# Performance work log

Measured on AMD Instinct MI355X. Metric: run time of the kernel, lower is better.

Reference implementation:

```python
import jax, jax.numpy as jnp
import numpy as np

STRIDE = (1, 1, 1)  # (h_stride, w_stride, d_stride)
# padding order in module: (left,right,up,down,forward,backward) -> h, w, d dims
PAD = ((1, 1), (1, 1), (1, 1))  # ((pad_left,pad_right) on h, (up,down) on w, (fwd,bwd) on d)


def setup_inputs() -> dict:
    key = jax.random.key(0)
    k1, k2, k3 = jax.random.split(key, 3)
    X = jax.random.normal(k1, (4, 32, 32, 64, 64), dtype=jnp.float32)        # (B, Cin, h, w, d)
    weight = jax.random.normal(k2, (64, 32, 3, 3, 3), dtype=jnp.float32) * 0.5  # (Cout, Cin, kh, kw, kd)
    bias = jax.random.normal(k3, (64,), dtype=jnp.float32) * 0.5
    return {"X": X, "weight": weight, "bias": bias}


def _conv3d(X, weight, bias):
    # cross-correlation conv3d, identical math to the nested-loop MAC in MyConv3d
    y = jax.lax.conv_general_dilated(
        X, weight,
        window_strides=STRIDE,
        padding=PAD,
        dimension_numbers=("NCHWD", "OIHWD", "NCHWD"),
    )
    return y + bias[None, :, None, None, None]


def reference(X, weight, bias):
    return _conv3d(X, weight, bias)
```

## Files before the change

### kernel.cpp

```cpp
#include <hip/hip_runtime.h>
#include <hip/hip_bf16.h>

typedef __attribute__((ext_vector_type(8))) short bf16x8;
typedef __attribute__((ext_vector_type(4))) float f32x4;
typedef __attribute__((ext_vector_type(4))) unsigned int u32x4;

#define B_N   4
#define C_IN  32
#define C_OUT 64
#define S_H   32
#define S_W   64
#define S_D   64
#define HWD   (S_H * S_W * S_D)

#define WPK_USHORTS     (4 * 28 * 64 * 8)
#define WS_NEEDED       ((size_t)WPK_USHORTS * 2 + 64)

__device__ __forceinline__ ushort f2bf(float f) {
    unsigned u = __builtin_bit_cast(unsigned, f);
    unsigned r = (u + 0x7FFFu + ((u >> 16) & 1u)) >> 16;
    return (ushort)r;
}

__device__ __forceinline__ unsigned cvt_pk(float lo, float hi) {
    unsigned r;
    asm("v_cvt_pk_bf16_f32 %0, %1, %2" : "=v"(r) : "v"(lo), "v"(hi));
    return r;
}

typedef const __attribute__((address_space(1))) unsigned int* dma_gptr;
typedef __attribute__((address_space(3))) unsigned int* dma_lptr;

__device__ __forceinline__ void dma16(const void* g, void* l) {
    __builtin_amdgcn_global_load_lds((dma_gptr)g, (dma_lptr)l, 16, 0, 0);
}

__device__ __forceinline__ void pin_load(float& dst, const float* p) {
    asm volatile("global_load_dword %0, %1, off" : "=v"(dst) : "v"(p));
}

__global__ __launch_bounds__(256) void pack_w_kernel(
    const float* __restrict__ Wt, ushort* __restrict__ Wpk, float* __restrict__ Zpf)
{
    int idx = blockIdx.x * 256 + threadIdx.x;
    int cic = idx / 1792;
    int r   = idx - cic * 1792;
    int tap = r >> 6;
    int co  = r & 63;
    bf16x8 pk;
    #pragma unroll
    for (int j = 0; j < 8; ++j)
        pk[j] = (tap < 27) ? (short)f2bf(Wt[((long)co * C_IN + cic * 8 + j) * 27 + tap])
                           : (short)0;
    *((bf16x8*)Wpk + idx) = pk;
    if (blockIdx.x == 0 && threadIdx.x < 16) Zpf[threadIdx.x] = 0.f;
}

__global__ __launch_bounds__(256, 2) void conv3d_fused_kernel(
    const float* __restrict__ X, const ushort* __restrict__ Wpk,
    const float* __restrict__ Zpf,
    const float* __restrict__ bias, float* __restrict__ out)
{
    __shared__ ushort Xs[1188 * 8];
    __shared__ ushort Ws[1792 * 8];

    const int tid  = threadIdx.x;
    const int lane = tid & 63;
    const int wave = tid >> 6;
    const int nl   = lane & 15;
    const int quad = lane >> 4;

    const int blk = blockIdx.x;
    const int wt  = blk & 15;
    const int h   = (blk >> 4) & 31;
    const int b   = blk >> 9;
    const int w0  = wt * 4;

    const int cs = ((blk >> 3) + (blk >> 8)) & 3;

    const float* xb[5];
    int adv[5];
    #pragma unroll
    for (int k = 0; k < 5; ++k) {
        int s = tid + k * 256;
        xb[k] = Zpf; adv[k] = 0;
        if (s < 1188) {
            int hh   = s / 396;
            int r0   = s - hh * 396;
            int ww   = r0 / 66;
            int dpos = r0 - ww * 66;
            int hp  = h - 1 + hh;
            int wp2 = w0 - 1 + ww;
            int dp  = dpos - 1;
            bool ok = (unsigned)hp < S_H && (unsigned)wp2 < S_W && (unsigned)dp < S_D;
            if (ok) {
                xb[k]  = X + ((((long)b * C_IN) * S_H + hp) * S_W + wp2) * S_D + dp;
                adv[k] = HWD;
            }
        }
    }

    int a_off[7], b_off[7];
    #pragma unroll
    for (int tg = 0; tg < 7; ++tg) {
        int tap = tg * 4 + quad;
        int tb  = tap < 27 ? tap : 0;
        int kh = tb / 9;
        int r9 = tb - kh * 9;
        int kw = r9 / 3;
        int kd = r9 - kw * 3;
        a_off[tg] = (tap * 64 + nl) * 8;
        b_off[tg] = (((kh * 6 + kw + wave) * 66) + kd + nl) * 8;
    }

    float bs[16];
    #pragma unroll
    for (int mi = 0; mi < 4; ++mi)
        #pragma unroll
        for (int r = 0; r < 4; ++r)
            bs[mi * 4 + r] = bias[mi * 16 + quad * 4 + r];

    f32x4 acc[16];
    #pragma unroll
    for (int i = 0; i < 16; ++i) acc[i] = (f32x4){0.f, 0.f, 0.f, 0.f};

    float xv[5][8];

    #pragma unroll
    for (int k = 0; k < 5; ++k) {
        int s = tid + k * 256;
        if (s < 1188) {
            #pragma unroll
            for (int j = 0; j < 8; ++j)
                pin_load(xv[k][j], xb[k] + (long)(cs * 8 + j) * adv[k]);
        }
    }
    __builtin_amdgcn_sched_barrier(0);
    {
        const ushort* src = Wpk + (long)cs * 1792 * 8;
        #pragma unroll
        for (int k = 0; k < 7; ++k) {
            int s = tid + k * 256;
            dma16(src + s * 8, &Ws[s * 8]);
        }
    }
    __builtin_amdgcn_sched_barrier(0);
    asm volatile("s_waitcnt vmcnt(7)" ::: "memory");
    __builtin_amdgcn_sched_barrier(0);
    #pragma unroll
    for (int k = 0; k < 5; ++k) {
        int s = tid + k * 256;
        if (s < 1188) {
            u32x4 pk;
            #pragma unroll
            for (int j = 0; j < 4; ++j)
                pk[j] = cvt_pk(xv[k][2 * j], xv[k][2 * j + 1]);
            *(u32x4*)&Xs[s * 8] = pk;
        }
    }

    for (int cic = 0; cic < 4; ++cic) {
        __syncthreads();

        const int cn = (cic + 1 + cs) & 3;
        if (cic < 3) {
            #pragma unroll
            for (int k = 0; k < 5; ++k) {
                int s = tid + k * 256;
                if (s < 1188) {
                    #pragma unroll
                    for (int j = 0; j < 8; ++j)
                        pin_load(xv[k][j], xb[k] + (long)(cn * 8 + j) * adv[k]);
                }
            }
        }
        __builtin_amdgcn_sched_barrier(0);

        #pragma unroll
        for (int tg = 0; tg < 7; ++tg) {
            bf16x8 af[4], bf[4];
            #pragma unroll
            for (int mi = 0; mi < 4; ++mi)
                af[mi] = *(const bf16x8*)&Ws[a_off[tg] + mi * 128];
            #pragma unroll
            for (int dt = 0; dt < 4; ++dt)
                bf[dt] = *(const bf16x8*)&Xs[b_off[tg] + dt * 128];
            __builtin_amdgcn_s_setprio(1);
            #pragma unroll
            for (int mi = 0; mi < 4; ++mi)
                #pragma unroll
                for (int dt = 0; dt < 4; ++dt)
                    acc[mi * 4 + dt] = __builtin_amdgcn_mfma_f32_16x16x32_bf16(
                        af[mi], bf[dt], acc[mi * 4 + dt], 0, 0, 0);
            __builtin_amdgcn_s_setprio(0);
        }

        if (cic < 3) {
            __syncthreads();
            asm volatile("s_waitcnt vmcnt(0)" ::: "memory");
            __builtin_amdgcn_sched_barrier(0);

            {
                const ushort* src = Wpk + (long)cn * 1792 * 8;
                #pragma unroll
                for (int k = 0; k < 7; ++k) {
                    int s = tid + k * 256;
                    dma16(src + s * 8, &Ws[s * 8]);
                }
            }
            #pragma unroll
            for (int k = 0; k < 5; ++k) {
                int s = tid + k * 256;
                if (s < 1188) {
                    u32x4 pk;
                    #pragma unroll
                    for (int j = 0; j < 4; ++j)
                        pk[j] = cvt_pk(xv[k][2 * j], xv[k][2 * j + 1]);
                    *(u32x4*)&Xs[s * 8] = pk;
                }
            }
        }
    }

    const int w = w0 + wave;
    #pragma unroll
    for (int mi = 0; mi < 4; ++mi) {
        #pragma unroll
        for (int dt = 0; dt < 4; ++dt) {
            f32x4 a = acc[mi * 4 + dt];
            int d0 = dt * 16 + nl;
            #pragma unroll
            for (int r = 0; r < 4; ++r) {
                int co = mi * 16 + quad * 4 + r;
                out[(((long)(b * C_OUT + co) * S_H + h) * S_W + w) * S_D + d0]
                    = a[r] + bs[mi * 4 + r];
            }
        }
    }
}

__global__ __launch_bounds__(256) void conv3d_mfma_fallback(
    const float* __restrict__ X, const float* __restrict__ Wt,
    const float* __restrict__ bias, float* __restrict__ out)
{
    __shared__ ushort Xs[3 * 6 * 66 * 8];
    __shared__ ushort Ws[28 * 64 * 8];

    const int tid  = threadIdx.x;
    const int lane = tid & 63;
    const int wave = tid >> 6;
    const int nl   = lane & 15;
    const int quad = lane >> 4;
    const int co_base = wave * 16;

    const int blk = blockIdx.x;
    const int wt  = blk & 15;
    const int h   = (blk >> 4) & 31;
    const int b   = blk >> 9;
    const int w0  = wt * 4;

    float bs[4];
    #pragma unroll
    for (int r = 0; r < 4; ++r) bs[r] = bias[co_base + quad * 4 + r];

    f32x4 acc[16];
    #pragma unroll
    for (int i = 0; i < 16; ++i) acc[i] = (f32x4){0.f, 0.f, 0.f, 0.f};

    for (int cic = 0; cic < 4; ++cic) {
        __syncthreads();
        for (int s = tid; s < 64 * 27; s += 256) {
            int co = s / 27;
            int t  = s - co * 27;
            const float* wp = Wt + ((long)co * C_IN + cic * 8) * 27 + t;
            bf16x8 pk;
            #pragma unroll
            for (int j = 0; j < 8; ++j) pk[j] = (short)f2bf(wp[j * 27]);
            *(bf16x8*)&Ws[(t * 64 + co) * 8] = pk;
        }
        for (int s = tid; s < 64; s += 256) {
            bf16x8 z;
            #pragma unroll
            for (int j = 0; j < 8; ++j) z[j] = 0;
            *(bf16x8*)&Ws[(27 * 64 + s) * 8] = z;
        }
        for (int s = tid; s < 1188; s += 256) {
            int hh   = s / 396;
            int r0   = s - hh * 396;
            int ww   = r0 / 66;
            int dpos = r0 - ww * 66;
            int hp = h - 1 + hh;
            int wp2 = w0 - 1 + ww;
            int dp = dpos - 1;
            bool ok = (unsigned)hp < S_H && (unsigned)wp2 < S_W && (unsigned)dp < S_D;
            int hc = min(max(hp, 0), S_H - 1);
            int wc = min(max(wp2, 0), S_W - 1);
            int dc = min(max(dp, 0), S_D - 1);
            const float* xp = X + (((long)(b * C_IN + cic * 8) * S_H + hc) * S_W + wc) * S_D + dc;
            bf16x8 pk;
            #pragma unroll
            for (int j = 0; j < 8; ++j) {
                float v = xp[(long)j * HWD];
                pk[j] = ok ? (short)f2bf(v) : (short)0;
            }
            *(bf16x8*)&Xs[s * 8] = pk;
        }
        __syncthreads();

        #pragma unroll
        for (int tg = 0; tg < 7; ++tg) {
            int tap = tg * 4 + quad;
            bf16x8 afrag = *(const bf16x8*)&Ws[(tap * 64 + co_base + nl) * 8];
            int tb = tap < 27 ? tap : 0;
            int kh = tb / 9;
            int r9 = tb - kh * 9;
            int kw = r9 / 3;
            int kd = r9 - kw * 3;
            int bbase = ((kh * 6 + kw) * 66 + kd + nl) * 8;
            #pragma unroll
            for (int wi = 0; wi < 4; ++wi) {
                #pragma unroll
                for (int dt = 0; dt < 4; ++dt) {
                    bf16x8 bfrag = *(const bf16x8*)&Xs[bbase + wi * (66 * 8) + dt * (16 * 8)];
                    acc[wi * 4 + dt] = __builtin_amdgcn_mfma_f32_16x16x32_bf16(
                        afrag, bfrag, acc[wi * 4 + dt], 0, 0, 0);
                }
            }
        }
    }

    #pragma unroll
    for (int wi = 0; wi < 4; ++wi) {
        int w = w0 + wi;
        #pragma unroll
        for (int dt = 0; dt < 4; ++dt) {
            int d0 = dt * 16 + nl;
            f32x4 a = acc[wi * 4 + dt];
            #pragma unroll
            for (int r = 0; r < 4; ++r) {
                int co = co_base + quad * 4 + r;
                out[(((long)(b * C_OUT + co) * S_H + h) * S_W + w) * S_D + d0] = a[r] + bs[r];
            }
        }
    }
}

extern "C" void kernel_launch(void* const* d_in, const int* in_sizes, int n_in,
                              void* d_out, int out_size, void* d_ws, size_t ws_size,
                              hipStream_t stream) {
    const float* X    = (const float*)d_in[0];
    const float* Wt   = (const float*)d_in[1];
    const float* bias = (const float*)d_in[2];
    float* out = (float*)d_out;

    if (ws_size >= WS_NEEDED) {
        ushort* Wpk = (ushort*)d_ws;
        float*  Zpf = (float*)((char*)d_ws + (size_t)WPK_USHORTS * 2);
        pack_w_kernel<<<dim3(28),   dim3(256), 0, stream>>>(Wt, Wpk, Zpf);
        conv3d_fused_kernel<<<dim3(2048), dim3(256), 0, stream>>>(X, Wpk, Zpf, bias, out);
    } else {
        conv3d_mfma_fallback<<<dim3(2048), dim3(256), 0, stream>>>(X, Wt, bias, out);
    }
}
```

Before: 225.8 us.

## Pre-pack X into padded bf16 layout and run LDS-free flat conv kernel

Adds a pack_x kernel that converts X to bf16 with 8-channel vectors and zero-padded depth, stored in workspace, and a new conv kernel that loads MFMA operands straight from global memory (relying on cache) with no shared-memory staging or barriers. The fused kernel also loses its channel-chunk staggering and setprio hints. This trades an extra full pass over X (read fp32, write bf16) and depends on a large workspace, for a simpler main loop without syncs. If the workspace is too small it falls back to the old path.

```diff
diff --git a/kernel.cpp b/kernel.cpp
--- a/kernel.cpp
+++ b/kernel.cpp
@@ -5,7 +5,6 @@
 typedef __attribute__((ext_vector_type(4))) float f32x4;
 typedef __attribute__((ext_vector_type(4))) unsigned int u32x4;
 
-#define B_N   4
 #define C_IN  32
 #define C_OUT 64
 #define S_H   32
@@ -13,8 +12,15 @@
 #define S_D   64
 #define HWD   (S_H * S_W * S_D)
 
-#define WPK_USHORTS     (4 * 28 * 64 * 8)
-#define WS_NEEDED       ((size_t)WPK_USHORTS * 2 + 64)
+#define WPK_BYTES   (4 * 28 * 64 * 8 * 2)
+#define ZPF_OFF     WPK_BYTES
+#define XPK_OFF     (WPK_BYTES + 64)
+#define XPK_SITES   (4 * 4 * 32 * 64 * 66)
+#define XPK_BYTES   ((size_t)XPK_SITES * 16)
+#define XPK_CIC_STR (4 * 32 * 64 * 66 * 16)
+#define WS_FLAT     ((size_t)XPK_OFF + XPK_BYTES)
+#define WS_FUSED    ((size_t)WPK_BYTES + 64)
+#define WZERO_OFF   (27 * 1024)
 
 __device__ __forceinline__ ushort f2bf(float f) {
     unsigned u = __builtin_bit_cast(unsigned, f);
@@ -56,6 +62,119 @@
     if (blockIdx.x == 0 && threadIdx.x < 16) Zpf[threadIdx.x] = 0.f;
 }
 
+__global__ __launch_bounds__(256) void pack_x_kernel(
+    const float* __restrict__ X, ushort* __restrict__ Xpk)
+{
+    int idx = blockIdx.x * 256 + threadIdx.x;
+    int dd  = idx % 66;
+    int t   = idx / 66;
+    int w   = t & 63; t >>= 6;
+    int h   = t & 31; t >>= 5;
+    int b   = t & 3;
+    int cic = (t >> 2) & 3;
+    int dp  = dd - 1;
+    bool ok = (unsigned)dp < (unsigned)S_D;
+    int dc  = ok ? dp : 0;
+    const float* xp = X + (((long)(b * C_IN + cic * 8) * S_H + h) * S_W + w) * S_D + dc;
+    u32x4 pk;
+    #pragma unroll
+    for (int j = 0; j < 4; ++j) {
+        float lo = ok ? xp[(long)(2 * j)     * HWD] : 0.f;
+        float hi = ok ? xp[(long)(2 * j + 1) * HWD] : 0.f;
+        pk[j] = cvt_pk(lo, hi);
+    }
+    *((u32x4*)Xpk + idx) = pk;
+}
+
+__global__ __launch_bounds__(256, 2) void conv3d_flat_kernel(
+    const ushort* __restrict__ Xpk, const ushort* __restrict__ Wpk,
+    const float* __restrict__ bias, float* __restrict__ out)
+{
+    const int tid  = threadIdx.x;
+    const int lane = tid & 63;
+    const int wave = tid >> 6;
+    const int nl   = lane & 15;
+    const int quad = lane >> 4;
+
+    const int blk = blockIdx.x;
+    const int wt  = blk & 15;
+    const int h   = (blk >> 4) & 31;
+    const int b   = blk >> 9;
+    const int w0  = wt * 4;
+
+    const char* pb[7];
+    int         advb[7];
+    #pragma unroll
+    for (int tg = 0; tg < 7; ++tg) {
+        int tap = tg * 4 + quad;
+        int tb  = tap < 27 ? tap : 0;
+        int kh = tb / 9, r9 = tb - kh * 9;
+        int kw = r9 / 3, kd = r9 - kw * 3;
+        int hp = h - 1 + kh;
+        int wp = w0 + wave - 1 + kw;
+        bool ok = (unsigned)hp < S_H && (unsigned)wp < S_W;
+        if (ok) {
+            pb[tg] = (const char*)Xpk +
+                     ((((long)b * S_H + hp) * S_W + wp) * 66 + nl + kd) * 16;
+            advb[tg] = XPK_CIC_STR;
+        } else {
+            pb[tg] = (const char*)Wpk + WZERO_OFF + nl * 16;
+            advb[tg] = 0;
+        }
+    }
+    const char* pa = (const char*)Wpk + quad * 1024 + nl * 16;
+
+    float bs[16];
+    #pragma unroll
+    for (int mi = 0; mi < 4; ++mi)
+        #pragma unroll
+        for (int r = 0; r < 4; ++r)
+            bs[mi * 4 + r] = bias[mi * 16 + quad * 4 + r];
+
+    f32x4 acc[16];
+    #pragma unroll
+    for (int i = 0; i < 16; ++i) acc[i] = (f32x4){0.f, 0.f, 0.f, 0.f};
+
+    #pragma unroll 1
+    for (int cic = 0; cic < 4; ++cic) {
+        #pragma unroll
+        for (int tg = 0; tg < 7; ++tg) {
+            bf16x8 af[4], bf[4];
+            #pragma unroll
+            for (int mi = 0; mi < 4; ++mi)
+                af[mi] = *(const bf16x8*)(pa + mi * 256);
+            #pragma unroll
+            for (int dt = 0; dt < 4; ++dt)
+                bf[dt] = *(const bf16x8*)(pb[tg] + dt * 256);
+            #pragma unroll
+            for (int mi = 0; mi < 4; ++mi)
+                #pragma unroll
+                for (int dt = 0; dt < 4; ++dt)
+                    acc[mi * 4 + dt] = __builtin_amdgcn_mfma_f32_16x16x32_bf16(
+                        af[mi], bf[dt], acc[mi * 4 + dt], 0, 0, 0);
+            pa += 4096;
+        }
+        #pragma unroll
+        for (int tg = 0; tg < 7; ++tg) pb[tg] += advb[tg];
+    }
+
+    const int w = w0 + wave;
+    #pragma unroll
+    for (int mi = 0; mi < 4; ++mi) {
+        #pragma unroll
+        for (int dt = 0; dt < 4; ++dt) {
+            f32x4 a = acc[mi * 4 + dt];
+            int d0 = dt * 16 + nl;
+            #pragma unroll
+            for (int r = 0; r < 4; ++r) {
+                int co = mi * 16 + quad * 4 + r;
+                out[(((long)(b * C_OUT + co) * S_H + h) * S_W + w) * S_D + d0]
+                    = a[r] + bs[mi * 4 + r];
+            }
+        }
+    }
+}
+
 __global__ __launch_bounds__(256, 2) void conv3d_fused_kernel(
     const float* __restrict__ X, const ushort* __restrict__ Wpk,
     const float* __restrict__ Zpf,
@@ -75,8 +194,6 @@
     const int h   = (blk >> 4) & 31;
     const int b   = blk >> 9;
     const int w0  = wt * 4;
-
-    const int cs = ((blk >> 3) + (blk >> 8)) & 3;
 
     const float* xb[5];
     int adv[5];
@@ -132,17 +249,14 @@
         if (s < 1188) {
             #pragma unroll
             for (int j = 0; j < 8; ++j)
-                pin_load(xv[k][j], xb[k] + (long)(cs * 8 + j) * adv[k]);
+                pin_load(xv[k][j], xb[k] + (long)j * adv[k]);
         }
     }
     __builtin_amdgcn_sched_barrier(0);
-    {
-        const ushort* src = Wpk + (long)cs * 1792 * 8;
-        #pragma unroll
-        for (int k = 0; k < 7; ++k) {
-            int s = tid + k * 256;
-            dma16(src + s * 8, &Ws[s * 8]);
-        }
+    #pragma unroll
+    for (int k = 0; k < 7; ++k) {
+        int s = tid + k * 256;
+        dma16(Wpk + s * 8, &Ws[s * 8]);
     }
     __builtin_amdgcn_sched_barrier(0);
     asm volatile("s_waitcnt vmcnt(7)" ::: "memory");
@@ -162,7 +276,6 @@
     for (int cic = 0; cic < 4; ++cic) {
         __syncthreads();
 
-        const int cn = (cic + 1 + cs) & 3;
         if (cic < 3) {
             #pragma unroll
             for (int k = 0; k < 5; ++k) {
@@ -170,7 +283,8 @@
                 if (s < 1188) {
                     #pragma unroll
                     for (int j = 0; j < 8; ++j)
-                        pin_load(xv[k][j], xb[k] + (long)(cn * 8 + j) * adv[k]);
+                        pin_load(xv[k][j],
+                                 xb[k] + (long)((cic + 1) * 8 + j) * adv[k]);
                 }
             }
         }
@@ -185,23 +299,20 @@
             #pragma unroll
             for (int dt = 0; dt < 4; ++dt)
                 bf[dt] = *(const bf16x8*)&Xs[b_off[tg] + dt * 128];
-            __builtin_amdgcn_s_setprio(1);
             #pragma unroll
             for (int mi = 0; mi < 4; ++mi)
                 #pragma unroll
                 for (int dt = 0; dt < 4; ++dt)
                     acc[mi * 4 + dt] = __builtin_amdgcn_mfma_f32_16x16x32_bf16(
                         af[mi], bf[dt], acc[mi * 4 + dt], 0, 0, 0);
-            __builtin_amdgcn_s_setprio(0);
         }
 
         if (cic < 3) {
             __syncthreads();
             asm volatile("s_waitcnt vmcnt(0)" ::: "memory");
             __builtin_amdgcn_sched_barrier(0);
-
             {
-                const ushort* src = Wpk + (long)cn * 1792 * 8;
+                const ushort* src = Wpk + (long)(cic + 1) * 1792 * 8;
                 #pragma unroll
                 for (int k = 0; k < 7; ++k) {
                     int s = tid + k * 256;
@@ -353,10 +464,17 @@
     const float* bias = (const float*)d_in[2];
     float* out = (float*)d_out;
 
-    if (ws_size >= WS_NEEDED) {
+    if (ws_size >= WS_FLAT) {
         ushort* Wpk = (ushort*)d_ws;
-        float*  Zpf = (float*)((char*)d_ws + (size_t)WPK_USHORTS * 2);
+        float*  Zpf = (float*)((char*)d_ws + ZPF_OFF);
+        ushort* Xpk = (ushort*)((char*)d_ws + XPK_OFF);
         pack_w_kernel<<<dim3(28),   dim3(256), 0, stream>>>(Wt, Wpk, Zpf);
+        pack_x_kernel<<<dim3(8448), dim3(256), 0, stream>>>(X, Xpk);
+        conv3d_flat_kernel<<<dim3(2048), dim3(256), 0, stream>>>(Xpk, Wpk, bias, out);
+    } else if (ws_size >= WS_FUSED) {
+        ushort* Wpk = (ushort*)d_ws;
+        float*  Zpf = (float*)((char*)d_ws + ZPF_OFF);
+        pack_w_kernel<<<dim3(28), dim3(256), 0, stream>>>(Wt, Wpk, Zpf);
         conv3d_fused_kernel<<<dim3(2048), dim3(256), 0, stream>>>(X, Wpk, Zpf, bias, out);
     } else {
         conv3d_mfma_fallback<<<dim3(2048), dim3(256), 0, stream>>>(X, Wt, bias, out);
```

Measured after the change: 272.8 us. 1.21x slower.
